# Performance work log

Hardware: AMD Instinct MI355X
Metric: run time of the kernel (lower is better)

The kernel has to match this reference:

```python
import jax, jax.numpy as jnp
import numpy as np

B, S, H, I, E, K = 4, 2048, 1024, 2048, 8, 2


def setup_inputs() -> dict:
    key = jax.random.key(0)
    ks = jax.random.split(key, 5)
    scale = 0.02  # typical init scale for transformer weights
    return {
        "hidden_states": jax.random.normal(ks[0], (B, S, H), jnp.float32),
        "router_w": jax.random.normal(ks[1], (E, H), jnp.float32) * scale,
        "gate_w": jax.random.normal(ks[2], (E, I, H), jnp.float32) * scale,
        "up_w": jax.random.normal(ks[3], (E, I, H), jnp.float32) * scale,
        "down_w": jax.random.normal(ks[4], (E, H, I), jnp.float32) * scale,
    }


def reference(hidden_states, router_w, gate_w, up_w, down_w):
    b, s, h = hidden_states.shape
    e, top_k = router_w.shape[0], K
    flat = hidden_states.reshape(-1, h)            # [T, H]
    t = flat.shape[0]

    # Router: top-k softmax with renormalized weights.
    logits = flat @ router_w.T                     # [T, E]
    probs = jax.nn.softmax(logits, axis=-1)
    topk_probs, topk_idx = jax.lax.top_k(probs, top_k)   # [T, K]
    w = topk_probs / jnp.sum(topk_probs, axis=-1, keepdims=True)

    # Per-token combine weight for each expert (0 if not selected).
    combine = jnp.zeros((t, e), flat.dtype).at[
        jnp.arange(t)[:, None], topk_idx
    ].add(w)                                       # [T, E]

    # Expert SwiGLU FFNs; non-selected tokens get zero combine weight,
    # which matches the masked gather/scatter-add of the original.
    out = jnp.zeros_like(flat)
    for ei in range(e):  # small fixed expert loop
        hidden = jax.nn.silu(flat @ gate_w[ei].T) * (flat @ up_w[ei].T)  # [T, I]
        out = out + combine[:, ei:ei + 1] * (hidden @ down_w[ei].T)      # [T, H]

    output = out.reshape(b, s, h)

    # Aux routing stats.
    one_hot = jax.nn.one_hot(topk_idx, e, dtype=flat.dtype)  # [T, K, E]
    expert_frac = jnp.sum(one_hot, axis=(0, 1)) / (t * top_k)
    avg_prob = jnp.mean(probs, axis=0)
    return output, expert_frac, avg_prob, logits, probs
```

## Files before the change

kernel.cpp:

```cpp
#include <hip/hip_runtime.h>
#include <hip/hip_bf16.h>
#include <cstdio>
#include <cstdint>

#define T_TOK   8192
#define H_DIM   1024
#define I_DIM   2048
#define E_NUM   8
#define BM      128
#define BK2     32
#define PADMAX  17408
#define MAX_TILES 136
#define HB      32
#define PAIRS_PER_HB (T_TOK*2/HB)

#define OUT_FRAC  8388608
#define OUT_AVG   8388616
#define OUT_LOG   8388624
#define OUT_PROB  8454160

typedef short short8v __attribute__((ext_vector_type(8)));
typedef float f32x4   __attribute__((ext_vector_type(4)));
typedef unsigned int u32x4 __attribute__((ext_vector_type(4)));

#define AS1 __attribute__((address_space(1)))
#define AS3 __attribute__((address_space(3)))
__device__ __forceinline__ void gload16(const void* g, void* l){
  __builtin_amdgcn_global_load_lds((const AS1 void*)g, (AS3 void*)l, 16, 0, 0);
}

#define WAITV6_BAR asm volatile("s_waitcnt vmcnt(6)\n\ts_barrier" ::: "memory")
#define WAITV4_BAR asm volatile("s_waitcnt vmcnt(4)\n\ts_barrier" ::: "memory")
#define WAITV0_BAR asm volatile("s_waitcnt vmcnt(0)\n\ts_barrier" ::: "memory")
#define SBAR  __builtin_amdgcn_s_barrier()
#define SCHED0 __builtin_amdgcn_sched_barrier(0)

__device__ __forceinline__ uint32_t f2bf(float f){
  union { float f; uint32_t u; } v; v.f = f;
  return (v.u + 0x7FFFu + ((v.u >> 16) & 1u)) >> 16;
}
__device__ __forceinline__ uint32_t pack2(float a, float b){
  return f2bf(a) | (f2bf(b) << 16);
}
__device__ __forceinline__ float bflo(uint32_t u){ union{uint32_t u;float f;}v; v.u = u<<16; return v.f; }
__device__ __forceinline__ float bfhi(uint32_t u){ union{uint32_t u;float f;}v; v.u = u & 0xFFFF0000u; return v.f; }

#define NWB  (E_NUM*I_DIM*H_DIM/2048)
__global__ __launch_bounds__(256) void convert3_kernel(
    const float* __restrict__ gw, const float* __restrict__ uw,
    const float* __restrict__ dw,
    ushort* __restrict__ gwb, ushort* __restrict__ uwb, ushort* __restrict__ dwb){
  const int b = blockIdx.x;
  const float* src; ushort* dst; size_t base;
  if (b < NWB)        { src = gw; dst = gwb; base = (size_t)b * 2048; }
  else if (b < 2*NWB) { src = uw; dst = uwb; base = (size_t)(b-NWB) * 2048; }
  else                { src = dw; dst = dwb; base = (size_t)(b-2*NWB) * 2048; }
  size_t i = base + (size_t)threadIdx.x * 8;
  f32x4 f0 = *(const f32x4*)(src + i);
  f32x4 f1 = *(const f32x4*)(src + i + 4);
  u32x4 o;
  o.x = pack2(f0.x, f0.y); o.y = pack2(f0.z, f0.w);
  o.z = pack2(f1.x, f1.y); o.w = pack2(f1.z, f1.w);
  *(u32x4*)(dst + i) = o;
}

__global__ __launch_bounds__(256) void router_kernel(const float* __restrict__ x,
    const float* __restrict__ rw, float* __restrict__ out,
    int* __restrict__ pe, float* __restrict__ pw, float* __restrict__ avg_part,
    ushort* __restrict__ xb){
  __shared__ float s_rw[E_NUM * H_DIM];
  __shared__ float s_avg[E_NUM];
  const int tid = threadIdx.x;
  for (int i = tid; i < E_NUM*H_DIM/4; i += 256)
    ((float4*)s_rw)[i] = ((const float4*)rw)[i];
  if (tid < E_NUM) s_avg[tid] = 0.f;
  __syncthreads();
  const int lane = tid & 63;
  const int t = blockIdx.x * 4 + (tid >> 6);
  float acc[E_NUM];
  #pragma unroll
  for (int e=0;e<E_NUM;e++) acc[e] = 0.f;
  const float* xr = x + (size_t)t * H_DIM;
  ushort* xbr = xb + (size_t)t * H_DIM;
  for (int c=0;c<H_DIM/64;c++){
    float xv = xr[c*64 + lane];
    xbr[c*64 + lane] = (ushort)f2bf(xv);
    #pragma unroll
    for (int e=0;e<E_NUM;e++) acc[e] += xv * s_rw[e*H_DIM + c*64 + lane];
  }
  #pragma unroll
  for (int e=0;e<E_NUM;e++){
    #pragma unroll
    for (int off=32; off; off>>=1) acc[e] += __shfl_xor(acc[e], off);
  }
  if (lane == 0){
    float m = acc[0];
    #pragma unroll
    for (int e=1;e<E_NUM;e++) m = fmaxf(m, acc[e]);
    float p[E_NUM]; float s = 0.f;
    #pragma unroll
    for (int e=0;e<E_NUM;e++){ p[e] = __expf(acc[e]-m); s += p[e]; }
    float inv = 1.f/s;
    #pragma unroll
    for (int e=0;e<E_NUM;e++) p[e] *= inv;
    float* lg = out + OUT_LOG  + (size_t)t*E_NUM;
    float* pr = out + OUT_PROB + (size_t)t*E_NUM;
    #pragma unroll
    for (int e=0;e<E_NUM;e++){ lg[e] = acc[e]; pr[e] = p[e]; }
    #pragma unroll
    for (int e=0;e<E_NUM;e++) atomicAdd(&s_avg[e], p[e]);
    int e1 = 0; float p1 = p[0];
    #pragma unroll
    for (int e=1;e<E_NUM;e++) if (p[e] > p1){ p1 = p[e]; e1 = e; }
    int e2 = -1; float p2 = -1.f;
    #pragma unroll
    for (int e=0;e<E_NUM;e++) if (e != e1 && p[e] > p2){ p2 = p[e]; e2 = e; }
    float rs = 1.f/(p1+p2);
    pe[2*t]   = e1; pw[2*t]   = p1*rs;
    pe[2*t+1] = e2; pw[2*t+1] = p2*rs;
  }
  __syncthreads();
  if (tid < E_NUM) avg_part[blockIdx.x*E_NUM + tid] = s_avg[tid];
}

__global__ __launch_bounds__(256) void hist_kernel(const int* __restrict__ pe,
                                                   int* __restrict__ block_hist){
  __shared__ int h[E_NUM];
  if (threadIdx.x < E_NUM) h[threadIdx.x] = 0;
  __syncthreads();
  const int base = blockIdx.x * PAIRS_PER_HB;
  for (int i = threadIdx.x; i < PAIRS_PER_HB; i += 256)
    atomicAdd(&h[pe[base + i]], 1);
  __syncthreads();
  if (threadIdx.x < E_NUM) block_hist[blockIdx.x*E_NUM + threadIdx.x] = h[threadIdx.x];
}

__global__ __launch_bounds__(256) void offsets_kernel(const int* __restrict__ block_hist,
    const float* __restrict__ avg_part, int* __restrict__ block_base,
    int* __restrict__ tile_e, int* __restrict__ tile_r, int* __restrict__ hdr,
    int* __restrict__ s_tok, float* __restrict__ s_wt, float* __restrict__ out){
  __shared__ int counts[E_NUM];
  __shared__ float ap[256];
  const int tid = threadIdx.x;
  {
    const int e = tid & 7, chunk = tid >> 3;
    float s = 0.f;
    #pragma unroll 8
    for (int i = 0; i < 64; ++i)
      s += avg_part[(chunk*64 + i)*E_NUM + e];
    ap[tid] = s;
  }
  if (tid < E_NUM){
    int c = 0;
    #pragma unroll
    for (int b = 0; b < HB; ++b) c += block_hist[b*E_NUM + tid];
    counts[tid] = c;
  }
  __syncthreads();
  if (tid < E_NUM){
    float tot = 0.f;
    #pragma unroll
    for (int c = 0; c < 32; ++c) tot += ap[c*8 + tid];
    out[OUT_AVG  + tid] = tot * (1.f/8192.f);
    out[OUT_FRAC + tid] = (float)counts[tid] * (1.f/16384.f);
  }
  if (tid == 0){
    int base = 0, tt = 0;
    for (int e=0;e<E_NUM;e++){
      int run = base;
      for (int b=0;b<HB;b++){
        block_base[b*E_NUM + e] = run;
        run += block_hist[b*E_NUM + e];
      }
      int nt = (counts[e] + BM - 1) / BM;
      for (int i=0;i<nt;i++){ tile_e[tt] = e; tile_r[tt] = base + i*BM; tt++; }
      base += nt * BM;
    }
    hdr[0] = tt; hdr[1] = base;
  }
  for (int i = tid; i < PADMAX; i += blockDim.x){
    s_tok[i] = 0; s_wt[i] = 0.f;
  }
}

__global__ __launch_bounds__(256) void scatter_kernel(const int* __restrict__ pe,
    const float* __restrict__ pw, const int* __restrict__ block_base,
    int* __restrict__ s_tok, float* __restrict__ s_wt, int* __restrict__ slot_idx){
  __shared__ int h[E_NUM];
  if (threadIdx.x < E_NUM) h[threadIdx.x] = 0;
  __syncthreads();
  const int base = blockIdx.x * PAIRS_PER_HB;
  for (int i = threadIdx.x; i < PAIRS_PER_HB; i += 256){
    const int pi = base + i;
    const int e = pe[pi];
    const int r = atomicAdd(&h[e], 1);
    const int idx = block_base[blockIdx.x*E_NUM + e] + r;
    s_tok[idx] = pi >> 1;
    s_wt[idx]  = pw[pi];
    slot_idx[pi] = idx;
  }
}

__global__ __launch_bounds__(256, 2) void gateup_kernel(
    const ushort* __restrict__ xb, const ushort* __restrict__ gwb,
    const ushort* __restrict__ uwb, const int* __restrict__ s_tok,
    const int* __restrict__ tile_e, const int* __restrict__ tile_r,
    const int* __restrict__ hdr, ushort* __restrict__ h1)
{
  const int tile = blockIdx.y;
  if (tile >= hdr[0]) return;
  __shared__ short sA[3][BM*BK2];
  __shared__ short sG[3][BM*BK2];
  __shared__ short sU[3][BM*BK2];
  const int e = tile_e[tile];
  const int row0 = tile_r[tile];
  const int n0 = blockIdx.x * 128;
  const int tid = threadIdx.x, lane = tid & 63, wid = tid >> 6;

  const int srow = tid >> 2;
  const int scg  = ((tid & 3) ^ ((tid >> 3) & 3)) * 8;
  const int d0 = tid * 8, d1 = tid * 8 + 2048;
  const ushort* gA0 = xb  + (size_t)s_tok[row0 + srow]      * H_DIM + scg;
  const ushort* gA1 = xb  + (size_t)s_tok[row0 + srow + 64] * H_DIM + scg;
  const ushort* gG0 = gwb + ((size_t)e*I_DIM + n0 + srow)      * H_DIM + scg;
  const ushort* gG1 = gwb + ((size_t)e*I_DIM + n0 + srow + 64) * H_DIM + scg;
  const ushort* gU0 = uwb + ((size_t)e*I_DIM + n0 + srow)      * H_DIM + scg;
  const ushort* gU1 = uwb + ((size_t)e*I_DIM + n0 + srow + 64) * H_DIM + scg;

  const int wm = (wid >> 1) * 64, wn = (wid & 1) * 64;
  const int lr = lane & 15, q = lane >> 4;
  const int swc = (q ^ ((lr >> 1) & 3)) * 8;

  f32x4 accG[4][4] = {};
  f32x4 accU[4][4] = {};

  gload16(gA0,       &sA[0][d0]); gload16(gA1,       &sA[0][d1]);
  gload16(gG0,       &sG[0][d0]); gload16(gG1,       &sG[0][d1]);
  gload16(gU0,       &sU[0][d0]); gload16(gU1,       &sU[0][d1]);
  gload16(gA0 + BK2, &sA[1][d0]); gload16(gA1 + BK2, &sA[1][d1]);
  gload16(gG0 + BK2, &sG[1][d0]); gload16(gG1 + BK2, &sG[1][d1]);
  gload16(gU0 + BK2, &sU[1][d0]); gload16(gU1 + BK2, &sU[1][d1]);
  WAITV6_BAR;

  const int NK = H_DIM / BK2;
  int b0 = 0, b1 = 1, b2 = 2;
  for (int kt = 0; kt < NK; ++kt){
    short8v a_[4], bg_[4], bu_[4];
    #pragma unroll
    for (int mi=0;mi<4;mi++)
      a_[mi] = *(const short8v*)&sA[b0][(wm + mi*16 + lr)*BK2 + swc];
    #pragma unroll
    for (int ni=0;ni<4;ni++)
      bg_[ni] = *(const short8v*)&sG[b0][(wn + ni*16 + lr)*BK2 + swc];
    if (kt + 2 < NK){
      const int kof = (kt+2)*BK2;
      gload16(gA0 + kof, &sA[b2][d0]); gload16(gA1 + kof, &sA[b2][d1]);
      gload16(gG0 + kof, &sG[b2][d0]); gload16(gG1 + kof, &sG[b2][d1]);
    }
    SCHED0; SBAR; SCHED0;
    __builtin_amdgcn_s_setprio(1);
    #pragma unroll
    for (int ni=0;ni<4;ni++)
      #pragma unroll
      for (int mi=0;mi<4;mi++)
        accG[mi][ni] = __builtin_amdgcn_mfma_f32_16x16x32_bf16(a_[mi], bg_[ni], accG[mi][ni], 0,0,0);
    __builtin_amdgcn_s_setprio(0);
    SCHED0; SBAR;
    #pragma unroll
    for (int ni=0;ni<4;ni++)
      bu_[ni] = *(const short8v*)&sU[b0][(wn + ni*16 + lr)*BK2 + swc];
    if (kt + 2 < NK){
      const int kof = (kt+2)*BK2;
      gload16(gU0 + kof, &sU[b2][d0]); gload16(gU1 + kof, &sU[b2][d1]);
    }
    SCHED0; SBAR; SCHED0;
    __builtin_amdgcn_s_setprio(1);
    #pragma unroll
    for (int ni=0;ni<4;ni++)
      #pragma unroll
      for (int mi=0;mi<4;mi++)
        accU[mi][ni] = __builtin_amdgcn_mfma_f32_16x16x32_bf16(a_[mi], bu_[ni], accU[mi][ni], 0,0,0);
    __builtin_amdgcn_s_setprio(0);
    SCHED0;
    if (kt + 2 < NK)      WAITV6_BAR;
    else if (kt + 1 < NK) WAITV0_BAR;
    int tb = b0; b0 = b1; b1 = b2; b2 = tb;
  }

  #pragma unroll
  for (int mi=0;mi<4;mi++){
    #pragma unroll
    for (int r=0;r<4;r++){
      const int row = row0 + wm + mi*16 + q*4 + r;
      ushort* hp = h1 + (size_t)row * I_DIM + n0 + wn + lr;
      #pragma unroll
      for (int ni=0;ni<4;ni++){
        float g = accG[mi][ni][r], u = accU[mi][ni][r];
        float sv = g / (1.f + __expf(-g));
        hp[ni*16] = (ushort)f2bf(sv * u);
      }
    }
  }
}

__global__ __launch_bounds__(256, 3) void down_kernel(
    const ushort* __restrict__ h1, const ushort* __restrict__ dwb,
    const int* __restrict__ tile_e, const int* __restrict__ tile_r,
    const int* __restrict__ hdr, ushort* __restrict__ ds_out)
{
  const int tile = blockIdx.y;
  if (tile >= hdr[0]) return;
  __shared__ short sA[3][BM*BK2];
  __shared__ short sB[3][BM*BK2];
  const int e = tile_e[tile];
  const int row0 = tile_r[tile];
  const int n0 = blockIdx.x * 128;
  const int tid = threadIdx.x, lane = tid & 63, wid = tid >> 6;

  const int srow = tid >> 2;
  const int scg  = ((tid & 3) ^ ((tid >> 3) & 3)) * 8;
  const int d0 = tid * 8, d1 = tid * 8 + 2048;
  const ushort* gA0 = h1  + (size_t)(row0 + srow)      * I_DIM + scg;
  const ushort* gA1 = h1  + (size_t)(row0 + srow + 64) * I_DIM + scg;
  const ushort* gB0 = dwb + ((size_t)e*H_DIM + n0 + srow)      * I_DIM + scg;
  const ushort* gB1 = dwb + ((size_t)e*H_DIM + n0 + srow + 64) * I_DIM + scg;

  const int wm = (wid >> 1) * 64, wn = (wid & 1) * 64;
  const int lr = lane & 15, q = lane >> 4;
  const int swc = (q ^ ((lr >> 1) & 3)) * 8;

  f32x4 acc[4][4] = {};

  gload16(gA0,       &sA[0][d0]); gload16(gA1,       &sA[0][d1]);
  gload16(gB0,       &sB[0][d0]); gload16(gB1,       &sB[0][d1]);
  gload16(gA0 + BK2, &sA[1][d0]); gload16(gA1 + BK2, &sA[1][d1]);
  gload16(gB0 + BK2, &sB[1][d0]); gload16(gB1 + BK2, &sB[1][d1]);
  WAITV4_BAR;

  const int NK = I_DIM / BK2;
  int b0 = 0, b1 = 1, b2 = 2;
  for (int kt = 0; kt < NK; ++kt){
    short8v a_[4], b_[4];
    #pragma unroll
    for (int mi=0;mi<4;mi++)
      a_[mi] = *(const short8v*)&sA[b0][(wm + mi*16 + lr)*BK2 + swc];
    #pragma unroll
    for (int ni=0;ni<2;ni++)
      b_[ni] = *(const short8v*)&sB[b0][(wn + ni*16 + lr)*BK2 + swc];
    if (kt + 2 < NK){
      const int kof = (kt+2)*BK2;
      gload16(gA0 + kof, &sA[b2][d0]); gload16(gA1 + kof, &sA[b2][d1]);
    }
    SCHED0; SBAR; SCHED0;
    __builtin_amdgcn_s_setprio(1);
    #pragma unroll
    for (int ni=0;ni<2;ni++)
      #pragma unroll
      for (int mi=0;mi<4;mi++)
        acc[mi][ni] = __builtin_amdgcn_mfma_f32_16x16x32_bf16(a_[mi], b_[ni], acc[mi][ni], 0,0,0);
    __builtin_amdgcn_s_setprio(0);
    SCHED0; SBAR;
    #pragma unroll
    for (int ni=2;ni<4;ni++)
      b_[ni] = *(const short8v*)&sB[b0][(wn + ni*16 + lr)*BK2 + swc];
    if (kt + 2 < NK){
      const int kof = (kt+2)*BK2;
      gload16(gB0 + kof, &sB[b2][d0]); gload16(gB1 + kof, &sB[b2][d1]);
    }
    SCHED0; SBAR; SCHED0;
    __builtin_amdgcn_s_setprio(1);
    #pragma unroll
    for (int ni=2;ni<4;ni++)
      #pragma unroll
      for (int mi=0;mi<4;mi++)
        acc[mi][ni] = __builtin_amdgcn_mfma_f32_16x16x32_bf16(a_[mi], b_[ni], acc[mi][ni], 0,0,0);
    __builtin_amdgcn_s_setprio(0);
    SCHED0;
    if (kt + 2 < NK)      WAITV4_BAR;
    else if (kt + 1 < NK) WAITV0_BAR;
    int tb = b0; b0 = b1; b1 = b2; b2 = tb;
  }

  #pragma unroll
  for (int mi=0;mi<4;mi++){
    #pragma unroll
    for (int r=0;r<4;r++){
      const int prow = row0 + wm + mi*16 + q*4 + r;
      ushort* op = ds_out + (size_t)prow * H_DIM + n0 + wn + lr;
      #pragma unroll
      for (int ni=0;ni<4;ni++)
        op[ni*16] = (ushort)f2bf(acc[mi][ni][r]);
    }
  }
}

__global__ __launch_bounds__(256) void combine_kernel(const ushort* __restrict__ ds_out,
    const int* __restrict__ slot_idx, const float* __restrict__ s_wt,
    float* __restrict__ out){
  const int t   = blockIdx.x * 2 + (threadIdx.x >> 7);
  const int col = (threadIdx.x & 127) * 8;
  const int s1 = slot_idx[2*t], s2 = slot_idx[2*t+1];
  const float w1 = s_wt[s1], w2 = s_wt[s2];
  const u32x4 a = *(const u32x4*)(ds_out + (size_t)s1 * H_DIM + col);
  const u32x4 b = *(const u32x4*)(ds_out + (size_t)s2 * H_DIM + col);
  float* op = out + (size_t)t * H_DIM + col;
  f32x4 o0, o1;
  o0.x = w1*bflo(a.x) + w2*bflo(b.x);
  o0.y = w1*bfhi(a.x) + w2*bfhi(b.x);
  o0.z = w1*bflo(a.y) + w2*bflo(b.y);
  o0.w = w1*bfhi(a.y) + w2*bfhi(b.y);
  o1.x = w1*bflo(a.z) + w2*bflo(b.z);
  o1.y = w1*bfhi(a.z) + w2*bfhi(b.z);
  o1.z = w1*bflo(a.w) + w2*bflo(b.w);
  o1.w = w1*bfhi(a.w) + w2*bfhi(b.w);
  *(f32x4*)op       = o0;
  *(f32x4*)(op + 4) = o1;
}

extern "C" void kernel_launch(void* const* d_in, const int* in_sizes, int n_in,
                              void* d_out, int out_size, void* d_ws, size_t ws_size,
                              hipStream_t stream){
  const float* x   = (const float*)d_in[0];
  const float* rw  = (const float*)d_in[1];
  const float* gw  = (const float*)d_in[2];
  const float* uw  = (const float*)d_in[3];
  const float* dwn = (const float*)d_in[4];
  float* out = (float*)d_out;

  char* w = (char*)d_ws;
  int*   hdr        = (int*)(w + 0);
  int*   tile_e     = (int*)(w + 256);
  int*   tile_r     = (int*)(w + 1280);
  int*   block_hist = (int*)(w + 2304);
  int*   block_base = (int*)(w + 3328);
  int*   s_tok      = (int*)(w + 8192);
  float* s_wt       = (float*)(w + 8192 + PADMAX*4);
  int*   pe         = (int*)(w + 8192 + PADMAX*8);
  float* pw         = (float*)(w + 8192 + PADMAX*8 + T_TOK*2*4);
  int*   slot_idx   = (int*)(w + 8192 + PADMAX*8 + T_TOK*2*8);
  float* avg_part   = (float*)(w + 8192 + PADMAX*8 + T_TOK*2*12);
  ushort* xb        = (ushort*)(w + 409600);
  ushort* h1        = (ushort*)(w + 409600 + (size_t)T_TOK*H_DIM*2);
  ushort* gwb       = (ushort*)(w + 409600 + (size_t)T_TOK*H_DIM*2 + (size_t)PADMAX*I_DIM*2);
  ushort* uwb       = gwb + (size_t)E_NUM*I_DIM*H_DIM;
  ushort* dwb       = uwb + (size_t)E_NUM*I_DIM*H_DIM;
  ushort* ds_out    = gwb;

  size_t need = 409600 + (size_t)T_TOK*H_DIM*2 + (size_t)PADMAX*I_DIM*2
              + 3ull * E_NUM*I_DIM*H_DIM * 2;
  if (ws_size < need){
    fprintf(stderr, "kernel_launch: ws too small (%zu < %zu)\n", ws_size, need);
    return;
  }

  convert3_kernel<<<3*NWB, 256, 0, stream>>>(gw, uw, dwn, gwb, uwb, dwb);
  router_kernel<<<T_TOK/4, 256, 0, stream>>>(x, rw, out, pe, pw, avg_part, xb);
  hist_kernel<<<HB, 256, 0, stream>>>(pe, block_hist);
  offsets_kernel<<<1, 256, 0, stream>>>(block_hist, avg_part, block_base,
                                        tile_e, tile_r, hdr, s_tok, s_wt, out);
  scatter_kernel<<<HB, 256, 0, stream>>>(pe, pw, block_base, s_tok, s_wt, slot_idx);
  gateup_kernel<<<dim3(I_DIM/128, MAX_TILES), 256, 0, stream>>>(xb, gwb, uwb, s_tok, tile_e, tile_r, hdr, h1);
  down_kernel<<<dim3(H_DIM/128, MAX_TILES), 256, 0, stream>>>(h1, dwb, tile_e, tile_r, hdr, ds_out);
  combine_kernel<<<T_TOK/2, 256, 0, stream>>>(ds_out, slot_idx, s_wt, out);
}
```

Measured before the change: 362.2 us.

## Merge weight conversion with router and collapse routing kernels into one

```diff
diff --git a/kernel.cpp b/kernel.cpp
--- a/kernel.cpp
+++ b/kernel.cpp
@@ -11,8 +11,6 @@
 #define BK2     32
 #define PADMAX  17408
 #define MAX_TILES 136
-#define HB      32
-#define PAIRS_PER_HB (T_TOK*2/HB)
 
 #define OUT_FRAC  8388608
 #define OUT_AVG   8388616
@@ -46,37 +44,43 @@
 __device__ __forceinline__ float bfhi(uint32_t u){ union{uint32_t u;float f;}v; v.u = u & 0xFFFF0000u; return v.f; }
 
 #define NWB  (E_NUM*I_DIM*H_DIM/2048)
-__global__ __launch_bounds__(256) void convert3_kernel(
+#define RB   (T_TOK/4)
+__global__ __launch_bounds__(256) void prep_kernel(
+    const float* __restrict__ x,  const float* __restrict__ rw,
     const float* __restrict__ gw, const float* __restrict__ uw,
     const float* __restrict__ dw,
-    ushort* __restrict__ gwb, ushort* __restrict__ uwb, ushort* __restrict__ dwb){
-  const int b = blockIdx.x;
-  const float* src; ushort* dst; size_t base;
-  if (b < NWB)        { src = gw; dst = gwb; base = (size_t)b * 2048; }
-  else if (b < 2*NWB) { src = uw; dst = uwb; base = (size_t)(b-NWB) * 2048; }
-  else                { src = dw; dst = dwb; base = (size_t)(b-2*NWB) * 2048; }
-  size_t i = base + (size_t)threadIdx.x * 8;
-  f32x4 f0 = *(const f32x4*)(src + i);
-  f32x4 f1 = *(const f32x4*)(src + i + 4);
-  u32x4 o;
-  o.x = pack2(f0.x, f0.y); o.y = pack2(f0.z, f0.w);
-  o.z = pack2(f1.x, f1.y); o.w = pack2(f1.z, f1.w);
-  *(u32x4*)(dst + i) = o;
-}
-
-__global__ __launch_bounds__(256) void router_kernel(const float* __restrict__ x,
-    const float* __restrict__ rw, float* __restrict__ out,
-    int* __restrict__ pe, float* __restrict__ pw, float* __restrict__ avg_part,
-    ushort* __restrict__ xb){
+    ushort* __restrict__ xb, ushort* __restrict__ gwb,
+    ushort* __restrict__ uwb, ushort* __restrict__ dwb,
+    float* __restrict__ out, int* __restrict__ pe, float* __restrict__ pw,
+    float* __restrict__ avg_part)
+{
   __shared__ float s_rw[E_NUM * H_DIM];
   __shared__ float s_avg[E_NUM];
+  const int b = blockIdx.x;
   const int tid = threadIdx.x;
+
+  if (b < 3*NWB){
+    const float* src; ushort* dst; size_t base;
+    if (b < NWB)        { src = gw; dst = gwb; base = (size_t)b * 2048; }
+    else if (b < 2*NWB) { src = uw; dst = uwb; base = (size_t)(b-NWB) * 2048; }
+    else                { src = dw; dst = dwb; base = (size_t)(b-2*NWB) * 2048; }
+    size_t i = base + (size_t)tid * 8;
+    f32x4 f0 = *(const f32x4*)(src + i);
+    f32x4 f1 = *(const f32x4*)(src + i + 4);
+    u32x4 o;
+    o.x = pack2(f0.x, f0.y); o.y = pack2(f0.z, f0.w);
+    o.z = pack2(f1.x, f1.y); o.w = pack2(f1.z, f1.w);
+    *(u32x4*)(dst + i) = o;
+    return;
+  }
+
+  const int rb = b - 3*NWB;
   for (int i = tid; i < E_NUM*H_DIM/4; i += 256)
     ((float4*)s_rw)[i] = ((const float4*)rw)[i];
   if (tid < E_NUM) s_avg[tid] = 0.f;
   __syncthreads();
   const int lane = tid & 63;
-  const int t = blockIdx.x * 4 + (tid >> 6);
+  const int t = rb * 4 + (tid >> 6);
   float acc[E_NUM];
   #pragma unroll
   for (int e=0;e<E_NUM;e++) acc[e] = 0.f;
@@ -120,28 +124,22 @@
     pe[2*t+1] = e2; pw[2*t+1] = p2*rs;
   }
   __syncthreads();
-  if (tid < E_NUM) avg_part[blockIdx.x*E_NUM + tid] = s_avg[tid];
-}
-
-__global__ __launch_bounds__(256) void hist_kernel(const int* __restrict__ pe,
-                                                   int* __restrict__ block_hist){
-  __shared__ int h[E_NUM];
-  if (threadIdx.x < E_NUM) h[threadIdx.x] = 0;
-  __syncthreads();
-  const int base = blockIdx.x * PAIRS_PER_HB;
-  for (int i = threadIdx.x; i < PAIRS_PER_HB; i += 256)
-    atomicAdd(&h[pe[base + i]], 1);
-  __syncthreads();
-  if (threadIdx.x < E_NUM) block_hist[blockIdx.x*E_NUM + threadIdx.x] = h[threadIdx.x];
-}
-
-__global__ __launch_bounds__(256) void offsets_kernel(const int* __restrict__ block_hist,
-    const float* __restrict__ avg_part, int* __restrict__ block_base,
+  if (tid < E_NUM) avg_part[rb*E_NUM + tid] = s_avg[tid];
+}
+
+__global__ __launch_bounds__(256) void route_kernel(const int* __restrict__ pe,
+    const float* __restrict__ pw, const float* __restrict__ avg_part,
     int* __restrict__ tile_e, int* __restrict__ tile_r, int* __restrict__ hdr,
-    int* __restrict__ s_tok, float* __restrict__ s_wt, float* __restrict__ out){
+    int* __restrict__ s_tok, float* __restrict__ s_wt, int* __restrict__ slot_idx,
+    float* __restrict__ out)
+{
   __shared__ int counts[E_NUM];
+  __shared__ int cur[E_NUM];
+  __shared__ int pad_off_s[E_NUM];
+  __shared__ int pad_end_s[E_NUM];
   __shared__ float ap[256];
   const int tid = threadIdx.x;
+  if (tid < E_NUM){ counts[tid] = 0; cur[tid] = 0; }
   {
     const int e = tid & 7, chunk = tid >> 3;
     float s = 0.f;
@@ -150,12 +148,9 @@
       s += avg_part[(chunk*64 + i)*E_NUM + e];
     ap[tid] = s;
   }
-  if (tid < E_NUM){
-    int c = 0;
-    #pragma unroll
-    for (int b = 0; b < HB; ++b) c += block_hist[b*E_NUM + tid];
-    counts[tid] = c;
-  }
+  __syncthreads();
+  for (int i = tid; i < T_TOK*2; i += 256)
+    atomicAdd(&counts[pe[i]], 1);
   __syncthreads();
   if (tid < E_NUM){
     float tot = 0.f;
@@ -167,37 +162,26 @@
   if (tid == 0){
     int base = 0, tt = 0;
     for (int e=0;e<E_NUM;e++){
-      int run = base;
-      for (int b=0;b<HB;b++){
-        block_base[b*E_NUM + e] = run;
-        run += block_hist[b*E_NUM + e];
-      }
+      pad_off_s[e] = base;
       int nt = (counts[e] + BM - 1) / BM;
       for (int i=0;i<nt;i++){ tile_e[tt] = e; tile_r[tt] = base + i*BM; tt++; }
       base += nt * BM;
+      pad_end_s[e] = base;
     }
     hdr[0] = tt; hdr[1] = base;
   }
-  for (int i = tid; i < PADMAX; i += blockDim.x){
-    s_tok[i] = 0; s_wt[i] = 0.f;
-  }
-}
-
-__global__ __launch_bounds__(256) void scatter_kernel(const int* __restrict__ pe,
-    const float* __restrict__ pw, const int* __restrict__ block_base,
-    int* __restrict__ s_tok, float* __restrict__ s_wt, int* __restrict__ slot_idx){
-  __shared__ int h[E_NUM];
-  if (threadIdx.x < E_NUM) h[threadIdx.x] = 0;
   __syncthreads();
-  const int base = blockIdx.x * PAIRS_PER_HB;
-  for (int i = threadIdx.x; i < PAIRS_PER_HB; i += 256){
-    const int pi = base + i;
-    const int e = pe[pi];
-    const int r = atomicAdd(&h[e], 1);
-    const int idx = block_base[blockIdx.x*E_NUM + e] + r;
-    s_tok[idx] = pi >> 1;
-    s_wt[idx]  = pw[pi];
-    slot_idx[pi] = idx;
+  for (int e=0;e<E_NUM;e++){
+    const int st = pad_off_s[e] + counts[e], en = pad_end_s[e];
+    for (int j = st + tid; j < en; j += 256){ s_tok[j] = 0; s_wt[j] = 0.f; }
+  }
+  for (int i = tid; i < T_TOK*2; i += 256){
+    const int e = pe[i];
+    const int r = atomicAdd(&cur[e], 1);
+    const int idx = pad_off_s[e] + r;
+    s_tok[idx] = i >> 1;
+    s_wt[idx]  = pw[i];
+    slot_idx[i] = idx;
   }
 }
 
@@ -431,8 +415,6 @@
   int*   hdr        = (int*)(w + 0);
   int*   tile_e     = (int*)(w + 256);
   int*   tile_r     = (int*)(w + 1280);
-  int*   block_hist = (int*)(w + 2304);
-  int*   block_base = (int*)(w + 3328);
   int*   s_tok      = (int*)(w + 8192);
   float* s_wt       = (float*)(w + 8192 + PADMAX*4);
   int*   pe         = (int*)(w + 8192 + PADMAX*8);
@@ -453,12 +435,11 @@
     return;
   }
 
-  convert3_kernel<<<3*NWB, 256, 0, stream>>>(gw, uw, dwn, gwb, uwb, dwb);
-  router_kernel<<<T_TOK/4, 256, 0, stream>>>(x, rw, out, pe, pw, avg_part, xb);
-  hist_kernel<<<HB, 256, 0, stream>>>(pe, block_hist);
-  offsets_kernel<<<1, 256, 0, stream>>>(block_hist, avg_part, block_base,
-                                        tile_e, tile_r, hdr, s_tok, s_wt, out);
-  scatter_kernel<<<HB, 256, 0, stream>>>(pe, pw, block_base, s_tok, s_wt, slot_idx);
+  prep_kernel<<<3*NWB + RB, 256, 0, stream>>>(x, rw, gw, uw, dwn,
+                                              xb, gwb, uwb, dwb,
+                                              out, pe, pw, avg_part);
+  route_kernel<<<1, 256, 0, stream>>>(pe, pw, avg_part, tile_e, tile_r, hdr,
+                                      s_tok, s_wt, slot_idx, out);
   gateup_kernel<<<dim3(I_DIM/128, MAX_TILES), 256, 0, stream>>>(xb, gwb, uwb, s_tok, tile_e, tile_r, hdr, h1);
   down_kernel<<<dim3(H_DIM/128, MAX_TILES), 256, 0, stream>>>(h1, dwb, tile_e, tile_r, hdr, ds_out);
   combine_kernel<<<T_TOK/2, 256, 0, stream>>>(ds_out, slot_idx, s_wt, out);
```

Result: slower. 391.1 us (+8.0%).
